# Performance work log

Measured on AMD Instinct MI355X. Metric: run time of the kernel, lower is better.

## Reference

```python
import jax, jax.numpy as jnp
import numpy as np


def _conv(x, w, pad, groups=1):
    # NCHW conv, OIHW weights, stride 1
    return jax.lax.conv_general_dilated(
        x, w, (1, 1), [(pad, pad), (pad, pad)],
        dimension_numbers=('NCHW', 'OIHW', 'NCHW'),
        feature_group_count=groups)


def setup_inputs() -> dict:
    key = jax.random.key(0)
    ks = jax.random.split(key, 16)
    b, c, h, w = 4, 64, 256, 256
    heads = 8
    s = 0.05
    inp = {
        'x': jax.random.normal(ks[0], (b, c, h, w), jnp.float32),
        # qkv 1x1 conv (with bias) then depthwise 3x3 (with bias)
        'w_qkv': jax.random.normal(ks[1], (3 * c, c, 1, 1), jnp.float32) * s,
        'b_qkv': jax.random.normal(ks[2], (3 * c,), jnp.float32) * s,
        'w_dw': jax.random.normal(ks[3], (3 * c, 1, 3, 3), jnp.float32) * s,
        'b_dw': jax.random.normal(ks[4], (3 * c,), jnp.float32) * s,
        # project_out 1x1 (with bias)
        'w_proj': jax.random.normal(ks[5], (c, c, 1, 1), jnp.float32) * s,
        'b_proj': jax.random.normal(ks[6], (c,), jnp.float32) * s,
        'temperature': jnp.ones((heads, 1, 1), jnp.float32),
        # V_MaskAttention.conv2: 1x1(no bias) -> BN -> 5x5 pad2(no bias)
        'w_m1': jax.random.normal(ks[7], (c, c, 1, 1), jnp.float32) * s,
        'bn_gamma': jnp.ones((c,), jnp.float32),
        'bn_beta': jnp.zeros((c,), jnp.float32),
        'bn_mean': jax.random.normal(ks[8], (c,), jnp.float32) * 0.1,
        'bn_var': jax.random.uniform(ks[9], (c,), jnp.float32, 0.5, 1.5),
        'w_m2': jax.random.normal(ks[10], (c, c, 5, 5), jnp.float32) * s,
    }
    return inp


def reference(x, w_qkv, b_qkv, w_dw, b_dw, w_proj, b_proj, temperature,
              w_m1, bn_gamma, bn_beta, bn_mean, bn_var, w_m2):
    b, c, h, w = x.shape
    heads = temperature.shape[0]

    # qkv conv1x1 + depthwise 3x3 (v chunk computed but unused, as in source)
    qkv = _conv(x, w_qkv, 0) + b_qkv[None, :, None, None]
    qkv = _conv(qkv, w_dw, 1, groups=3 * c) + b_dw[None, :, None, None]
    q, k, _ = jnp.split(qkv, 3, axis=1)

    # V_MaskAttention gated value path (BN in eval mode, eps=1e-5)
    y = _conv(x, w_m1, 0)
    y = (y - bn_mean[None, :, None, None]) * (
        bn_gamma[None, :, None, None]
        / jnp.sqrt(bn_var[None, :, None, None] + 1e-5)) + bn_beta[None, :, None, None]
    x2 = jax.nn.sigmoid(_conv(y, w_m2, 2))
    v = x + x * x2

    def heads_view(t):  # b,(head c),h,w -> b,head,c_head,hw
        return t.reshape(b, heads, c // heads, h * w)

    q = heads_view(q)
    k = heads_view(k)
    v = heads_view(v)

    # L2 normalize over spatial dim (torch F.normalize eps=1e-12)
    q = q / jnp.maximum(jnp.linalg.norm(q, axis=-1, keepdims=True), 1e-12)
    k = k / jnp.maximum(jnp.linalg.norm(k, axis=-1, keepdims=True), 1e-12)

    attn = jnp.einsum('bhcn,bhdn->bhcd', q, k) * temperature[None]  # [b,h,c',c']
    attn = jax.nn.softmax(attn, axis=-1)
    out = jnp.einsum('bhcd,bhdn->bhcn', attn, v).reshape(b, c, h, w)
    return _conv(out, w_proj, 0) + b_proj[None, :, None, None]
```

## Files before the change

### kernel.cpp

```cpp
#include <hip/hip_runtime.h>
#include <math.h>

#define B 4
#define C 64
#define NN 65536

typedef __attribute__((ext_vector_type(8))) short short8;
typedef __attribute__((ext_vector_type(4))) short short4b;
typedef __attribute__((ext_vector_type(4))) float f32x4;
typedef __attribute__((ext_vector_type(4))) unsigned int u32x4;

__device__ inline float bf2f(short s) {
  union { unsigned u; float f; } v; v.u = ((unsigned)(unsigned short)s) << 16; return v.f;
}
__device__ inline short f2bf(float f) {
  union { float f; unsigned u; } v; v.f = f;
  unsigned r = v.u + 0x7FFFu + ((v.u >> 16) & 1u);
  return (short)(r >> 16);
}
__device__ inline float lof(unsigned u) {
  union { unsigned u; float f; } v; v.u = u << 16; return v.f;
}
__device__ inline float hif(unsigned u) {
  union { unsigned u; float f; } v; v.u = u & 0xffff0000u; return v.f;
}

__global__ void k_prep1(const float* __restrict__ wqkv, const float* __restrict__ wm1,
    short* __restrict__ apk, short* __restrict__ apm, float* __restrict__ gram2) {
  for (int idx = blockIdx.x * 256 + threadIdx.x; idx < 20480; idx += 16384) {
    if (idx < 8192) {
      const int j = idx & 7, lane = (idx >> 3) & 63, mt = (idx >> 9) & 7, cc = idx >> 12;
      const int o = mt * 16 + (lane & 15), c = cc * 32 + (lane >> 4) * 8 + j;
      apk[idx] = f2bf(wqkv[o * 64 + c]);
    } else if (idx < 12288) {
      const int k = idx - 8192;
      const int j = k & 7, lane = (k >> 3) & 63, mt = (k >> 9) & 3, cc = k >> 11;
      const int o = mt * 16 + (lane & 15), c = cc * 32 + (lane >> 4) * 8 + j;
      apm[k] = f2bf(wm1[o * 64 + c]);
    } else {
      gram2[idx - 12288] = 0.f;
    }
  }
}

__global__ void k_prep2(const float* __restrict__ w2, short* __restrict__ apw2) {
  for (int idx = blockIdx.x * 256 + threadIdx.x; idx < 25 * 2 * 4 * 64 * 8; idx += 16384) {
    const int j = idx & 7, lane = (idx >> 3) & 63, mt = (idx >> 9) & 3,
              cc = (idx >> 11) & 1, t = idx >> 12;
    const int o = mt * 16 + (lane & 15);
    const int c = cc * 32 + (lane >> 4) * 8 + j;
    apw2[idx] = f2bf(w2[((size_t)o * 64 + c) * 25 + t]);
  }
}

__global__ __launch_bounds__(256) void k_xt(const float* __restrict__ x,
    short* __restrict__ x_t) {
  __shared__ short lds[256 * 72];
  const int b = blockIdx.x >> 8, n0 = (blockIdx.x & 255) << 8;
  const int t = threadIdx.x;
#pragma unroll 4
  for (int c = 0; c < 64; ++c)
    lds[t * 72 + c] = f2bf(x[((size_t)(b * 64 + c)) * NN + n0 + t]);
  __syncthreads();
  short* dst = x_t + ((size_t)(b * NN + n0)) * 64;
#pragma unroll
  for (int it = 0; it < 8; ++it) {
    const int idx = it * 256 + t;
    const int nl = idx >> 3, cb = idx & 7;
    *(short8*)(dst + (size_t)nl * 64 + cb * 8) = *(const short8*)(lds + nl * 72 + cb * 8);
  }
}

__global__ __launch_bounds__(256, 4) void k_qk1x1(const short* __restrict__ x_t,
    const short* __restrict__ apk, const float* __restrict__ bias,
    short* __restrict__ qk) {
  const int b = blockIdx.x >> 10, ntile = blockIdx.x & 1023;
  const int wave = threadIdx.x >> 6, lane = threadIdx.x & 63;
  const int quad = lane >> 4, l15 = lane & 15;
  const int n = ntile * 64 + wave * 16 + l15;
  f32x4 acc[8];
#pragma unroll
  for (int mt = 0; mt < 8; ++mt) acc[mt] = (f32x4){0.f, 0.f, 0.f, 0.f};
#pragma unroll
  for (int cc = 0; cc < 2; ++cc) {
    const short8 bf = *(const short8*)(x_t + ((size_t)(b * NN + n)) * 64 + cc * 32 + quad * 8);
#pragma unroll
    for (int mt = 0; mt < 8; ++mt) {
      const short8 af = *(const short8*)(apk + ((cc * 8 + mt) * 64 + lane) * 8);
      acc[mt] = __builtin_amdgcn_mfma_f32_16x16x32_bf16(af, bf, acc[mt], 0, 0, 0);
    }
  }
#pragma unroll
  for (int mt = 0; mt < 8; ++mt)
#pragma unroll
    for (int reg = 0; reg < 4; ++reg) {
      const int o = mt * 16 + quad * 4 + reg;
      qk[((size_t)(b * 128 + o)) * NN + n] = f2bf(acc[mt][reg] + bias[o]);
    }
}

__global__ __launch_bounds__(256, 3) void k_gram(const short* __restrict__ qk,
    const float* __restrict__ wdw, const float* __restrict__ bdw,
    float* __restrict__ gram2) {
  __shared__ float red[4][256];
  const int bh = blockIdx.x >> 6, chunk = blockIdx.x & 63;
  const int b = bh >> 3, h = bh & 7;
  const int wave = threadIdx.x >> 6, lane = threadIdx.x & 63;
  const int quad = lane >> 4, l15 = lane & 15;
  const int ch = (l15 < 8) ? (h * 8 + l15) : (64 + h * 8 + (l15 - 8));
  const short* plane = qk + ((size_t)(b * 128 + ch)) * NN;
  float wreg[9];
#pragma unroll
  for (int i = 0; i < 9; ++i) wreg[i] = wdw[ch * 9 + i];
  const float bias = bdw[ch];
  const int row = chunk * 4 + wave;
  const short* prow = plane + row * 256;
  u32x4 rb[3][8];
#pragma unroll
  for (int dy = 0; dy < 3; ++dy) {
    if (dy == 0 && row == 0) continue;
    if (dy == 2 && row == 255) continue;
    const short* pr = prow + (dy - 1) * 256 + quad * 8;
#pragma unroll
    for (int s = 0; s < 8; ++s)
      rb[dy][s] = *(const u32x4*)(pr + s * 32);
  }
  f32x4 acc = {0.f, 0.f, 0.f, 0.f};
#pragma unroll
  for (int s = 0; s < 8; ++s) {
    float a[8];
#pragma unroll
    for (int j = 0; j < 8; ++j) a[j] = bias;
#pragma unroll
    for (int dy = 0; dy < 3; ++dy) {
      if (dy == 0 && row == 0) continue;
      if (dy == 2 && row == 255) continue;
      const unsigned w0_ = rb[dy][s][0], w1_ = rb[dy][s][1],
                     w2_ = rb[dy][s][2], w3_ = rb[dy][s][3];
      float m[10];
      m[1] = lof(w0_); m[2] = hif(w0_);
      m[3] = lof(w1_); m[4] = hif(w1_);
      m[5] = lof(w2_); m[6] = hif(w2_);
      m[7] = lof(w3_); m[8] = hif(w3_);
      const unsigned A3 = (unsigned)__shfl((int)w3_, (lane - 16) & 63, 64);
      const unsigned A0 = (unsigned)__shfl((int)w0_, (lane + 16) & 63, 64);
      float m0q0 = 0.f, m9q3 = 0.f;
      if (s > 0) {
        const unsigned B3 = (unsigned)__shfl((int)rb[dy][s - 1][3], (lane + 48) & 63, 64);
        m0q0 = hif(B3);
      }
      if (s < 7) {
        const unsigned B0 = (unsigned)__shfl((int)rb[dy][s + 1][0], (lane - 48) & 63, 64);
        m9q3 = lof(B0);
      }
      m[0] = (quad == 0) ? m0q0 : hif(A3);
      m[9] = (quad == 3) ? m9q3 : lof(A0);
      const float W0 = wreg[dy * 3], W1 = wreg[dy * 3 + 1], W2 = wreg[dy * 3 + 2];
#pragma unroll
      for (int j = 0; j < 8; ++j)
        a[j] = fmaf(W2, m[j + 2], fmaf(W1, m[j + 1], fmaf(W0, m[j], a[j])));
    }
    short8 frag;
#pragma unroll
    for (int j = 0; j < 8; ++j) frag[j] = f2bf(a[j]);
    acc = __builtin_amdgcn_mfma_f32_16x16x32_bf16(frag, frag, acc, 0, 0, 0);
  }
#pragma unroll
  for (int reg = 0; reg < 4; ++reg)
    red[wave][(quad * 4 + reg) * 16 + l15] = acc[reg];
  __syncthreads();
  {
    const int e = threadIdx.x;
    const float s4 = red[0][e] + red[1][e] + red[2][e] + red[3][e];
    atomicAdd(&gram2[bh * 256 + e], s4);
  }
}

__global__ __launch_bounds__(256, 4) void k_m1_bn(const short* __restrict__ x_t,
    const short* __restrict__ apm, const float* __restrict__ gamma,
    const float* __restrict__ beta, const float* __restrict__ mean,
    const float* __restrict__ var, short* __restrict__ y_t) {
  __shared__ short lds[64 * 72];
  const int b = blockIdx.x >> 10, ntile = blockIdx.x & 1023;
  const int wave = threadIdx.x >> 6, lane = threadIdx.x & 63;
  const int quad = lane >> 4, l15 = lane & 15;
  const int n = ntile * 64 + wave * 16 + l15;
  f32x4 acc[4];
#pragma unroll
  for (int mt = 0; mt < 4; ++mt) acc[mt] = (f32x4){0.f, 0.f, 0.f, 0.f};
#pragma unroll
  for (int cc = 0; cc < 2; ++cc) {
    const short8 bf = *(const short8*)(x_t + ((size_t)(b * NN + n)) * 64 + cc * 32 + quad * 8);
#pragma unroll
    for (int mt = 0; mt < 4; ++mt) {
      const short8 af = *(const short8*)(apm + ((cc * 4 + mt) * 64 + lane) * 8);
      acc[mt] = __builtin_amdgcn_mfma_f32_16x16x32_bf16(af, bf, acc[mt], 0, 0, 0);
    }
  }
#pragma unroll
  for (int mt = 0; mt < 4; ++mt)
#pragma unroll
    for (int reg = 0; reg < 4; ++reg) {
      const int o = mt * 16 + quad * 4 + reg;
      const float sc = gamma[o] * rsqrtf(var[o] + 1e-5f);
      lds[(wave * 16 + l15) * 72 + o] = f2bf((acc[mt][reg] - mean[o]) * sc + beta[o]);
    }
  __syncthreads();
  short* dst = y_t + ((size_t)(b * NN + ntile * 64)) * 64;
#pragma unroll
  for (int it = 0; it < 2; ++it) {
    const int idx = it * 256 + threadIdx.x;
    const int lcol = idx >> 3, cb = idx & 7;
    *(short8*)(dst + (size_t)lcol * 64 + cb * 8) = *(const short8*)(lds + lcol * 72 + cb * 8);
  }
}

__global__ __launch_bounds__(256, 2) void k_conv5(const short* __restrict__ y_t,
    const short* __restrict__ apw2, const short* __restrict__ x_t,
    short* __restrict__ v_t) {
  __shared__ short slds[8 * 64 * 76];
  char* sb = (char*)slds;
  const int b = blockIdx.x >> 7;
  const int rg = (blockIdx.x >> 2) & 31, cg = blockIdx.x & 3;
  const int r0 = rg * 8, x0 = cg * 64;
  const int wave = threadIdx.x >> 6, lane = threadIdx.x & 63;
  const int quad = lane >> 4, l15 = lane & 15;
  f32x4 acc[4][2][4];
#pragma unroll
  for (int mt = 0; mt < 4; ++mt)
#pragma unroll
    for (int r = 0; r < 2; ++r)
#pragma unroll
      for (int nt = 0; nt < 4; ++nt) acc[mt][r][nt] = (f32x4){0.f, 0.f, 0.f, 0.f};
  for (int cc = 0; cc < 2; ++cc) {
    if (cc) __syncthreads();
    for (int idx = threadIdx.x; idx < 12 * 68 * 4; idx += 256) {
      const int rr = idx / 272, rem = idx - rr * 272;
      const int col = rem >> 2, cb = rem & 3;
      const int gr = r0 - 2 + rr, gc = x0 - 2 + col;
      short8 val = {0, 0, 0, 0, 0, 0, 0, 0};
      if (gr >= 0 && gr < 256 && gc >= 0 && gc < 256)
        val = *(const short8*)(y_t + ((size_t)(b * NN + gr * 256 + gc)) * 64 + cc * 32 + cb * 8);
      const int L = rr * 68 + col;
      *(short8*)(sb + ((L * 64 + cb * 16) ^ (((L >> 1) & 3) << 4))) = val;
    }
    __syncthreads();
    for (int t = 0; t < 25; ++t) {
      const int dy = t / 5 - 2, dx = t % 5 - 2;
      short8 a[4];
#pragma unroll
      for (int mt = 0; mt < 4; ++mt)
        a[mt] = *(const short8*)(apw2 + (((t * 2 + cc) * 4 + mt) * 64 + lane) * 8);
#pragma unroll
      for (int r = 0; r < 2; ++r) {
        const int rr = wave * 2 + r + 2 + dy;
#pragma unroll
        for (int nt = 0; nt < 4; ++nt) {
          const int L = rr * 68 + nt * 16 + l15 + 2 + dx;
          const short8 bf =
              *(const short8*)(sb + ((L * 64 + quad * 16) ^ (((L >> 1) & 3) << 4)));
#pragma unroll
          for (int mt = 0; mt < 4; ++mt)
            acc[mt][r][nt] =
                __builtin_amdgcn_mfma_f32_16x16x32_bf16(a[mt], bf, acc[mt][r][nt], 0, 0, 0);
        }
      }
    }
  }
  __syncthreads();
#pragma unroll
  for (int r = 0; r < 2; ++r) {
    const int lrow = wave * 2 + r;
    const int row = r0 + lrow;
#pragma unroll
    for (int nt = 0; nt < 4; ++nt) {
      const int lcol = nt * 16 + l15;
      const short* xp = x_t + ((size_t)(b * NN + row * 256 + x0 + lcol)) * 64 + quad * 4;
#pragma unroll
      for (int mt = 0; mt < 4; ++mt) {
        const short4b xv4 = *(const short4b*)(xp + mt * 16);
        short4b pk;
#pragma unroll
        for (int reg = 0; reg < 4; ++reg) {
          const float sg = 1.f / (1.f + __expf(-acc[mt][r][nt][reg]));
          pk[reg] = f2bf(bf2f(xv4[reg]) * (1.f + sg));
        }
        *(short4b*)(slds + (lrow * 64 + lcol) * 76 + mt * 16 + quad * 4) = pk;
      }
    }
  }
  __syncthreads();
#pragma unroll
  for (int it = 0; it < 16; ++it) {
    const int idx = it * 256 + threadIdx.x;
    const int cb = idx & 7, lcol = (idx >> 3) & 63, rr = idx >> 9;
    *(short8*)(v_t + ((size_t)(b * NN + (r0 + rr) * 256 + x0 + lcol)) * 64 + cb * 8) =
        *(const short8*)(slds + (rr * 64 + lcol) * 76 + cb * 8);
  }
}

__global__ __launch_bounds__(256) void k_attn_e(const float* __restrict__ gram2,
    const float* __restrict__ temp, const float* __restrict__ wproj,
    short* __restrict__ Epack) {
  __shared__ float attn[2048];
  const int t = threadIdx.x;
  {
    const int b = t >> 6, h = (t >> 3) & 7, c = t & 7;
    const float* g = gram2 + (b * 8 + h) * 256;
    const float qn = fmaxf(sqrtf(g[c * 16 + c]), 1e-12f);
    const float tp = temp[h];
    float row[8];
    float mx = -1e30f;
#pragma unroll
    for (int d = 0; d < 8; ++d) {
      const float kn = fmaxf(sqrtf(g[(8 + d) * 16 + (8 + d)]), 1e-12f);
      row[d] = g[c * 16 + 8 + d] / (qn * kn) * tp;
      mx = fmaxf(mx, row[d]);
    }
    float s = 0.f;
#pragma unroll
    for (int d = 0; d < 8; ++d) { row[d] = __expf(row[d] - mx); s += row[d]; }
    const float inv = 1.f / s;
#pragma unroll
    for (int d = 0; d < 8; ++d) attn[t * 8 + d] = row[d] * inv;
  }
  __syncthreads();
  for (int idx = t; idx < 16384; idx += 256) {
    const int j = idx & 7, lane = (idx >> 3) & 63, mt = (idx >> 9) & 3,
              cc = (idx >> 11) & 1, b = idx >> 12;
    const int o = mt * 16 + (lane & 15);
    const int cv = cc * 32 + (lane >> 4) * 8 + j;
    const int h = cv >> 3, d = cv & 7;
    float a = 0.f;
#pragma unroll
    for (int c2 = 0; c2 < 8; ++c2)
      a += wproj[o * 64 + h * 8 + c2] * attn[((b * 8 + h) * 8 + c2) * 8 + d];
    Epack[idx] = f2bf(a);
  }
}

__global__ __launch_bounds__(256, 4) void k_out(const short* __restrict__ v_t,
    const short* __restrict__ Epack, const float* __restrict__ bproj,
    float* __restrict__ out) {
  const int b = blockIdx.x >> 10, ntile = blockIdx.x & 1023;
  const int wave = threadIdx.x >> 6, lane = threadIdx.x & 63;
  const int quad = lane >> 4, l15 = lane & 15;
  const int n = ntile * 64 + wave * 16 + l15;
  f32x4 acc[4];
#pragma unroll
  for (int mt = 0; mt < 4; ++mt) acc[mt] = (f32x4){0.f, 0.f, 0.f, 0.f};
#pragma unroll
  for (int cc = 0; cc < 2; ++cc) {
    const short8 bf = *(const short8*)(v_t + ((size_t)(b * NN + n)) * 64 + cc * 32 + quad * 8);
#pragma unroll
    for (int mt = 0; mt < 4; ++mt) {
      const short8 af = *(const short8*)(Epack + (((b * 2 + cc) * 4 + mt) * 64 + lane) * 8);
      acc[mt] = __builtin_amdgcn_mfma_f32_16x16x32_bf16(af, bf, acc[mt], 0, 0, 0);
    }
  }
#pragma unroll
  for (int mt = 0; mt < 4; ++mt)
#pragma unroll
    for (int reg = 0; reg < 4; ++reg) {
      const int o = mt * 16 + quad * 4 + reg;
      out[((size_t)(b * 64 + o)) * NN + n] = acc[mt][reg] + bproj[o];
    }
}

extern "C" void kernel_launch(void* const* d_in, const int* in_sizes, int n_in,
                              void* d_out, int out_size, void* d_ws, size_t ws_size,
                              hipStream_t stream) {
  const float* x     = (const float*)d_in[0];
  const float* wqkv  = (const float*)d_in[1];
  const float* bqkv  = (const float*)d_in[2];
  const float* wdw   = (const float*)d_in[3];
  const float* bdw   = (const float*)d_in[4];
  const float* wproj = (const float*)d_in[5];
  const float* bproj = (const float*)d_in[6];
  const float* temp  = (const float*)d_in[7];
  const float* wm1   = (const float*)d_in[8];
  const float* gamma = (const float*)d_in[9];
  const float* beta  = (const float*)d_in[10];
  const float* mean  = (const float*)d_in[11];
  const float* var   = (const float*)d_in[12];
  const float* wm2   = (const float*)d_in[13];

  char* wsb = (char*)d_ws;
  short* qk    = (short*)(wsb);
  short* v_t   = (short*)(wsb);
  short* apw2  = (short*)(wsb + 33554432);
  short* x_t   = (short*)(wsb + 67108864);
  short* y_t   = (short*)(wsb + 100663296);
  float* gram2 = (float*)(wsb + 134217728);
  short* apk   = (short*)(wsb + 134217728 + 32768);
  short* apm   = (short*)(wsb + 134217728 + 49152);
  short* Epack = (short*)(wsb + 134217728 + 57344);
  float* out   = (float*)d_out;

  k_prep1<<<dim3(64), dim3(256), 0, stream>>>(wqkv, wm1, apk, apm, gram2);
  k_xt<<<dim3(1024), dim3(256), 0, stream>>>(x, x_t);
  k_qk1x1<<<dim3(4096), dim3(256), 0, stream>>>(x_t, apk, bqkv, qk);
  k_gram<<<dim3(2048), dim3(256), 0, stream>>>(qk, wdw, bdw, gram2);
  k_prep2<<<dim3(64), dim3(256), 0, stream>>>(wm2, apw2);
  k_m1_bn<<<dim3(4096), dim3(256), 0, stream>>>(x_t, apm, gamma, beta, mean, var, y_t);
  k_conv5<<<dim3(512), dim3(256), 0, stream>>>(y_t, apw2, x_t, v_t);
  k_attn_e<<<dim3(1), dim3(256), 0, stream>>>(gram2, temp, wproj, Epack);
  k_out<<<dim3(4096), dim3(256), 0, stream>>>(v_t, Epack, bproj, out);
}
```

Measured before the change: 305.0 us.

## Fold weight-prep kernels into main launches, tweak LDS padding and shuffles

Merges the two weight-packing kernels into extra blocks of k_xt and k_m1_bn, which removes two launches. It also changes the LDS row stride from 72 to 66 shorts, reduces the cross-lane shuffles in the depthwise gram kernel from four to two per step, and spreads the Epack construction in k_attn_e across 16 blocks. The 66-short stride breaks 16-byte alignment for the short8 LDS reads, so those may split into narrower accesses. Each attn block also recomputes the softmax redundantly.

```diff
diff --git a/kernel.cpp b/kernel.cpp
--- a/kernel.cpp
+++ b/kernel.cpp
@@ -25,49 +25,41 @@
   union { unsigned u; float f; } v; v.u = u & 0xffff0000u; return v.f;
 }
 
-__global__ void k_prep1(const float* __restrict__ wqkv, const float* __restrict__ wm1,
-    short* __restrict__ apk, short* __restrict__ apm, float* __restrict__ gram2) {
-  for (int idx = blockIdx.x * 256 + threadIdx.x; idx < 20480; idx += 16384) {
-    if (idx < 8192) {
-      const int j = idx & 7, lane = (idx >> 3) & 63, mt = (idx >> 9) & 7, cc = idx >> 12;
-      const int o = mt * 16 + (lane & 15), c = cc * 32 + (lane >> 4) * 8 + j;
-      apk[idx] = f2bf(wqkv[o * 64 + c]);
-    } else if (idx < 12288) {
-      const int k = idx - 8192;
-      const int j = k & 7, lane = (k >> 3) & 63, mt = (k >> 9) & 3, cc = k >> 11;
-      const int o = mt * 16 + (lane & 15), c = cc * 32 + (lane >> 4) * 8 + j;
-      apm[k] = f2bf(wm1[o * 64 + c]);
-    } else {
-      gram2[idx - 12288] = 0.f;
-    }
-  }
-}
-
-__global__ void k_prep2(const float* __restrict__ w2, short* __restrict__ apw2) {
-  for (int idx = blockIdx.x * 256 + threadIdx.x; idx < 25 * 2 * 4 * 64 * 8; idx += 16384) {
-    const int j = idx & 7, lane = (idx >> 3) & 63, mt = (idx >> 9) & 3,
-              cc = (idx >> 11) & 1, t = idx >> 12;
-    const int o = mt * 16 + (lane & 15);
-    const int c = cc * 32 + (lane >> 4) * 8 + j;
-    apw2[idx] = f2bf(w2[((size_t)o * 64 + c) * 25 + t]);
-  }
-}
-
 __global__ __launch_bounds__(256) void k_xt(const float* __restrict__ x,
-    short* __restrict__ x_t) {
-  __shared__ short lds[256 * 72];
+    short* __restrict__ x_t, const float* __restrict__ wqkv,
+    const float* __restrict__ wm1, short* __restrict__ apk,
+    short* __restrict__ apm, float* __restrict__ gram2) {
+  if (blockIdx.x >= 1024) {
+    const int bid = blockIdx.x - 1024;
+    for (int idx = bid * 256 + threadIdx.x; idx < 20480; idx += 16384) {
+      if (idx < 8192) {
+        const int j = idx & 7, lane = (idx >> 3) & 63, mt = (idx >> 9) & 7, cc = idx >> 12;
+        const int o = mt * 16 + (lane & 15), c = cc * 32 + (lane >> 4) * 8 + j;
+        apk[idx] = f2bf(wqkv[o * 64 + c]);
+      } else if (idx < 12288) {
+        const int k = idx - 8192;
+        const int j = k & 7, lane = (k >> 3) & 63, mt = (k >> 9) & 3, cc = k >> 11;
+        const int o = mt * 16 + (lane & 15), c = cc * 32 + (lane >> 4) * 8 + j;
+        apm[k] = f2bf(wm1[o * 64 + c]);
+      } else {
+        gram2[idx - 12288] = 0.f;
+      }
+    }
+    return;
+  }
+  __shared__ short lds[256 * 66];
   const int b = blockIdx.x >> 8, n0 = (blockIdx.x & 255) << 8;
   const int t = threadIdx.x;
 #pragma unroll 4
   for (int c = 0; c < 64; ++c)
-    lds[t * 72 + c] = f2bf(x[((size_t)(b * 64 + c)) * NN + n0 + t]);
+    lds[t * 66 + c] = f2bf(x[((size_t)(b * 64 + c)) * NN + n0 + t]);
   __syncthreads();
   short* dst = x_t + ((size_t)(b * NN + n0)) * 64;
 #pragma unroll
   for (int it = 0; it < 8; ++it) {
     const int idx = it * 256 + t;
     const int nl = idx >> 3, cb = idx & 7;
-    *(short8*)(dst + (size_t)nl * 64 + cb * 8) = *(const short8*)(lds + nl * 72 + cb * 8);
+    *(short8*)(dst + (size_t)nl * 64 + cb * 8) = *(const short8*)(lds + nl * 66 + cb * 8);
   }
 }
 
@@ -142,19 +134,21 @@
       m[3] = lof(w1_); m[4] = hif(w1_);
       m[5] = lof(w2_); m[6] = hif(w2_);
       m[7] = lof(w3_); m[8] = hif(w3_);
-      const unsigned A3 = (unsigned)__shfl((int)w3_, (lane - 16) & 63, 64);
-      const unsigned A0 = (unsigned)__shfl((int)w0_, (lane + 16) & 63, 64);
-      float m0q0 = 0.f, m9q3 = 0.f;
-      if (s > 0) {
-        const unsigned B3 = (unsigned)__shfl((int)rb[dy][s - 1][3], (lane + 48) & 63, 64);
-        m0q0 = hif(B3);
+      unsigned m0w, m9w;
+      if (s == 0) {
+        m0w = (unsigned)__shfl((int)w3_, (lane - 16) & 63, 64);
+      } else {
+        const unsigned w3sel = (quad == 3) ? rb[dy][s - 1][3] : w3_;
+        m0w = (unsigned)__shfl((int)w3sel, (lane - 16) & 63, 64);
       }
-      if (s < 7) {
-        const unsigned B0 = (unsigned)__shfl((int)rb[dy][s + 1][0], (lane - 48) & 63, 64);
-        m9q3 = lof(B0);
+      if (s == 7) {
+        m9w = (unsigned)__shfl((int)w0_, (lane + 16) & 63, 64);
+      } else {
+        const unsigned w0sel = (quad == 0) ? rb[dy][s + 1][0] : w0_;
+        m9w = (unsigned)__shfl((int)w0sel, (lane + 16) & 63, 64);
       }
-      m[0] = (quad == 0) ? m0q0 : hif(A3);
-      m[9] = (quad == 3) ? m9q3 : lof(A0);
+      m[0] = (s == 0 && quad == 0) ? 0.f : hif(m0w);
+      m[9] = (s == 7 && quad == 3) ? 0.f : lof(m9w);
       const float W0 = wreg[dy * 3], W1 = wreg[dy * 3 + 1], W2 = wreg[dy * 3 + 2];
 #pragma unroll
       for (int j = 0; j < 8; ++j)
@@ -179,8 +173,20 @@
 __global__ __launch_bounds__(256, 4) void k_m1_bn(const short* __restrict__ x_t,
     const short* __restrict__ apm, const float* __restrict__ gamma,
     const float* __restrict__ beta, const float* __restrict__ mean,
-    const float* __restrict__ var, short* __restrict__ y_t) {
-  __shared__ short lds[64 * 72];
+    const float* __restrict__ var, short* __restrict__ y_t,
+    const float* __restrict__ w2, short* __restrict__ apw2) {
+  if (blockIdx.x >= 4096) {
+    const int bid = blockIdx.x - 4096;
+    for (int idx = bid * 256 + threadIdx.x; idx < 25 * 2 * 4 * 64 * 8; idx += 16384) {
+      const int j = idx & 7, lane = (idx >> 3) & 63, mt = (idx >> 9) & 3,
+                cc = (idx >> 11) & 1, t = idx >> 12;
+      const int o = mt * 16 + (lane & 15);
+      const int c = cc * 32 + (lane >> 4) * 8 + j;
+      apw2[idx] = f2bf(w2[((size_t)o * 64 + c) * 25 + t]);
+    }
+    return;
+  }
+  __shared__ short lds[64 * 66];
   const int b = blockIdx.x >> 10, ntile = blockIdx.x & 1023;
   const int wave = threadIdx.x >> 6, lane = threadIdx.x & 63;
   const int quad = lane >> 4, l15 = lane & 15;
@@ -203,7 +209,7 @@
     for (int reg = 0; reg < 4; ++reg) {
       const int o = mt * 16 + quad * 4 + reg;
       const float sc = gamma[o] * rsqrtf(var[o] + 1e-5f);
-      lds[(wave * 16 + l15) * 72 + o] = f2bf((acc[mt][reg] - mean[o]) * sc + beta[o]);
+      lds[(wave * 16 + l15) * 66 + o] = f2bf((acc[mt][reg] - mean[o]) * sc + beta[o]);
     }
   __syncthreads();
   short* dst = y_t + ((size_t)(b * NN + ntile * 64)) * 64;
@@ -211,7 +217,7 @@
   for (int it = 0; it < 2; ++it) {
     const int idx = it * 256 + threadIdx.x;
     const int lcol = idx >> 3, cb = idx & 7;
-    *(short8*)(dst + (size_t)lcol * 64 + cb * 8) = *(const short8*)(lds + lcol * 72 + cb * 8);
+    *(short8*)(dst + (size_t)lcol * 64 + cb * 8) = *(const short8*)(lds + lcol * 66 + cb * 8);
   }
 }
 
@@ -325,7 +331,7 @@
     for (int d = 0; d < 8; ++d) attn[t * 8 + d] = row[d] * inv;
   }
   __syncthreads();
-  for (int idx = t; idx < 16384; idx += 256) {
+  for (int idx = blockIdx.x * 1024 + t; idx < (blockIdx.x + 1) * 1024; idx += 256) {
     const int j = idx & 7, lane = (idx >> 3) & 63, mt = (idx >> 9) & 3,
               cc = (idx >> 11) & 1, b = idx >> 12;
     const int o = mt * 16 + (lane & 15);
@@ -397,13 +403,12 @@
   short* Epack = (short*)(wsb + 134217728 + 57344);
   float* out   = (float*)d_out;
 
-  k_prep1<<<dim3(64), dim3(256), 0, stream>>>(wqkv, wm1, apk, apm, gram2);
-  k_xt<<<dim3(1024), dim3(256), 0, stream>>>(x, x_t);
+  k_xt<<<dim3(1088), dim3(256), 0, stream>>>(x, x_t, wqkv, wm1, apk, apm, gram2);
   k_qk1x1<<<dim3(4096), dim3(256), 0, stream>>>(x_t, apk, bqkv, qk);
   k_gram<<<dim3(2048), dim3(256), 0, stream>>>(qk, wdw, bdw, gram2);
-  k_prep2<<<dim3(64), dim3(256), 0, stream>>>(wm2, apw2);
-  k_m1_bn<<<dim3(4096), dim3(256), 0, stream>>>(x_t, apm, gamma, beta, mean, var, y_t);
+  k_m1_bn<<<dim3(4160), dim3(256), 0, stream>>>(x_t, apm, gamma, beta, mean, var, y_t,
+                                                wm2, apw2);
   k_conv5<<<dim3(512), dim3(256), 0, stream>>>(y_t, apw2, x_t, v_t);
-  k_attn_e<<<dim3(1), dim3(256), 0, stream>>>(gram2, temp, wproj, Epack);
+  k_attn_e<<<dim3(16), dim3(256), 0, stream>>>(gram2, temp, wproj, Epack);
   k_out<<<dim3(4096), dim3(256), 0, stream>>>(v_t, Epack, bproj, out);
 }
```

After: 293.5 us. 3.8% less time.
